# Kernel optimization log

Measured on AMD Instinct MI355X. Metric: run time of the kernel, lower is better.

Reference implementation:

```python
import jax, jax.numpy as jnp
import numpy as np
from functools import partial

DIM = 256
HEADS = 8
HEAD_DIM = DIM // HEADS
SCALES = (1, 2, 4)
B, H, W = 1, 64, 64


def _dwconv3x3(x, w, b):
    # x: (B,C,H,W), w: (C,1,3,3) depthwise, b: (C,)
    y = jax.lax.conv_general_dilated(
        x, w, window_strides=(1, 1), padding='SAME',
        feature_group_count=x.shape[1],
        dimension_numbers=('NCHW', 'OIHW', 'NCHW'))
    return y + b[None, :, None, None]


def _pwconv(x, w, b):
    # 1x1 conv: x (B,C,H,W), w (O,C), b (O,)
    return jnp.einsum('bchw,oc->bohw', x, w) + b[None, :, None, None]


def _avg_pool(x, s):
    Bb, C, Hh, Ww = x.shape
    return x.reshape(Bb, C, Hh // s, s, Ww // s, s).mean(axis=(3, 5))


def setup_inputs() -> dict:
    key = jax.random.key(0)
    ks = jax.random.split(key, 9)
    sc = 0.05
    return {
        'x': jax.random.normal(ks[0], (B, DIM, H, W), dtype=jnp.float32),
        'dw_w': jax.random.normal(ks[1], (3, DIM, 1, 3, 3), dtype=jnp.float32) * sc,
        'dw_b': jax.random.normal(ks[2], (3, DIM), dtype=jnp.float32) * sc,
        'pw_w': jax.random.normal(ks[3], (3, 3 * DIM, DIM), dtype=jnp.float32) * sc,
        'pw_b': jax.random.normal(ks[4], (3, 3 * DIM), dtype=jnp.float32) * sc,
        'pos_w': jax.random.normal(ks[5], (3, DIM, 1, 3, 3), dtype=jnp.float32) * sc,
        'pos_b': jax.random.normal(ks[6], (3, DIM), dtype=jnp.float32) * sc,
        'fusion_w': jax.random.normal(ks[7], (DIM, 3 * DIM), dtype=jnp.float32) * sc,
        'fusion_b': jax.random.normal(ks[8], (DIM,), dtype=jnp.float32) * sc,
    }


def reference(x, dw_w, dw_b, pw_w, pw_b, pos_w, pos_b, fusion_w, fusion_b):
    Bb, C, Hh, Ww = x.shape
    outputs = []
    for i, scale in enumerate(SCALES):
        xs = _avg_pool(x, scale) if scale > 1 else x
        # ConvQKV
        x_dw = _dwconv3x3(xs, dw_w[i], dw_b[i])
        qkv = _pwconv(x_dw, pw_w[i], pw_b[i])
        q, k, v = jnp.split(qkv, 3, axis=1)
        pos = _dwconv3x3(xs, pos_w[i], pos_b[i])
        q = q + pos
        k = k + pos
        Hs, Ws = xs.shape[2], xs.shape[3]
        Ns = Hs * Ws
        # (B, heads, head_dim, N)
        q = q.reshape(Bb, HEADS, HEAD_DIM, Ns)
        k = k.reshape(Bb, HEADS, HEAD_DIM, Ns)
        v = v.reshape(Bb, HEADS, HEAD_DIM, Ns)
        attn = jnp.einsum('bhdn,bhdm->bhnm', q, k) / (HEAD_DIM ** 0.5)
        attn = jax.nn.softmax(attn, axis=-1)
        out = jnp.einsum('bhnm,bhdm->bhdn', attn, v)  # (B,h,hd,N)
        out = out.reshape(Bb, C, Hs, Ws)
        if scale > 1:
            out = jax.image.resize(out, (Bb, C, Hh, Ww), method='bilinear')
        outputs.append(out)
    cat = jnp.concatenate(outputs, axis=1)  # (B, 3C, H, W)
    return jnp.einsum('bchw,oc->bohw', cat, fusion_w) + fusion_b[None, :, None, None]
```

## Files before the change

kernel.cpp:

```cpp
#include <hip/hip_runtime.h>
#include <math.h>

#define DIM 256
#define HEADS 8
#define HD 32
#define QSCALE 0.25504526770295183f

typedef __attribute__((ext_vector_type(8))) short bf16x8;
typedef __attribute__((ext_vector_type(4))) float f32x4;

#if __has_builtin(__builtin_amdgcn_exp2f)
#define EXP2(x) __builtin_amdgcn_exp2f(x)
#else
#define EXP2(x) __expf((x) * 0.6931471805599453f)
#endif

__device__ __forceinline__ unsigned short f2bf(float f) {
  unsigned int u = __float_as_uint(f);
  unsigned int r = u + 0x7fff + ((u >> 16) & 1);
  return (unsigned short)(r >> 16);
}
__device__ __forceinline__ float bf2f(unsigned short u) {
  return __uint_as_float(((unsigned int)u) << 16);
}


__global__ __launch_bounds__(256) void prep_kernel(const float* __restrict__ x,
    const float* __restrict__ pw_w, const float* __restrict__ fus_w,
    float* __restrict__ xs2, float* __restrict__ xs4,
    unsigned short* __restrict__ Wb, unsigned short* __restrict__ Wf) {
  const int gx = blockIdx.x, t = threadIdx.x;
  if (gx < 1024) {
    int id = gx * 256 + t;
    int c = id >> 10, n = id & 1023;
    int y = (n >> 5) << 1, x0 = (n & 31) << 1;
    const float* b = x + c * 4096 + y * 64 + x0;
    xs2[id] = (b[0] + b[1] + b[64] + b[65]) * 0.25f;
  } else if (gx < 1280) {
    int id = (gx - 1024) * 256 + t;
    int c = id >> 8, n = id & 255;
    int y = (n >> 4) << 2, x0 = (n & 15) << 2;
    const float* b = x + c * 4096 + y * 64 + x0;
    float s = 0.f;
    #pragma unroll
    for (int dy = 0; dy < 4; ++dy)
      #pragma unroll
      for (int dx = 0; dx < 4; ++dx) s += b[dy * 64 + dx];
    xs4[id] = s * 0.0625f;
  } else if (gx < 1424) {
    int lid = (gx - 1280) * 256 + t;
    int fb = lid >> 5, l = lid & 31;
    int scale = fb / 384, bs = fb - scale * 384;
    int rtile = bs >> 3, kchunk = bs & 7;
    int r = scale * 768 + rtile * 16 + (l & 7) * 2;
    int k = kchunk * 32 + (l >> 3) * 8;
    const float* s0 = pw_w + (size_t)r * 256 + k;
    float4 u0 = *(const float4*)(s0);
    float4 u1 = *(const float4*)(s0 + 4);
    float4 u2 = *(const float4*)(s0 + 256);
    float4 u3 = *(const float4*)(s0 + 260);
    unsigned short* d = Wb + (size_t)fb * 512 + l * 16;
    ushort4 a0 = {f2bf(u0.x), f2bf(u0.y), f2bf(u0.z), f2bf(u0.w)};
    ushort4 a1 = {f2bf(u1.x), f2bf(u1.y), f2bf(u1.z), f2bf(u1.w)};
    ushort4 a2 = {f2bf(u2.x), f2bf(u2.y), f2bf(u2.z), f2bf(u2.w)};
    ushort4 a3 = {f2bf(u3.x), f2bf(u3.y), f2bf(u3.z), f2bf(u3.w)};
    *(ushort4*)(d)      = a0;
    *(ushort4*)(d + 4)  = a1;
    *(ushort4*)(d + 8)  = a2;
    *(ushort4*)(d + 12) = a3;
  } else {
    int lid = (gx - 1424) * 256 + t;
    int fb = lid >> 5, l = lid & 31;
    int rtile = fb / 24, kchunk = fb - rtile * 24;
    int r = rtile * 16 + (l & 7) * 2;
    int k = kchunk * 32 + (l >> 3) * 8;
    const float* s0 = fus_w + (size_t)r * 768 + k;
    float4 u0 = *(const float4*)(s0);
    float4 u1 = *(const float4*)(s0 + 4);
    float4 u2 = *(const float4*)(s0 + 768);
    float4 u3 = *(const float4*)(s0 + 772);
    unsigned short* d = Wf + (size_t)fb * 512 + l * 16;
    ushort4 a0 = {f2bf(u0.x), f2bf(u0.y), f2bf(u0.z), f2bf(u0.w)};
    ushort4 a1 = {f2bf(u1.x), f2bf(u1.y), f2bf(u1.z), f2bf(u1.w)};
    ushort4 a2 = {f2bf(u2.x), f2bf(u2.y), f2bf(u2.z), f2bf(u2.w)};
    ushort4 a3 = {f2bf(u3.x), f2bf(u3.y), f2bf(u3.z), f2bf(u3.w)};
    *(ushort4*)(d)      = a0;
    *(ushort4*)(d + 4)  = a1;
    *(ushort4*)(d + 8)  = a2;
    *(ushort4*)(d + 12) = a3;
  }
}

__global__ __launch_bounds__(256) void dwt_kernel(const float* __restrict__ x,
    const float* __restrict__ xs2, const float* __restrict__ xs4,
    const float* __restrict__ dw_w, const float* __restrict__ dw_b,
    const float* __restrict__ pos_w, const float* __restrict__ pos_b,
    unsigned short* __restrict__ xdwT, unsigned short* __restrict__ posTc) {
  __shared__ __align__(16) unsigned short lds1[32][40];
  int b = blockIdx.x;
  const float* src;
  int lgHs, wo, soff;
  if (b < 1024)      { src = x;   lgHs = 6; wo = 0; soff = 0; }
  else if (b < 1280) { b -= 1024; src = xs2; lgHs = 5; wo = 1; soff = 1048576; }
  else               { b -= 1280; src = xs4; lgHs = 4; wo = 2; soff = 1310720; }
  const int c0 = (b & 7) * 32;
  const int n0 = (b >> 3) * 32;
  const int Hs = 1 << lgHs;
  const int Ns = Hs * Hs;
  const int t = threadIdx.x;
  const int cl = t >> 3;
  const int c = c0 + cl;
  const int nb = (t & 7) * 4;
  const float* w1 = dw_w + wo * 2304 + c * 9;
  const float* w2 = pos_w + wo * 2304 + c * 9;
  const float b1 = dw_b[wo * 256 + c], b2 = pos_b[wo * 256 + c];
  const int gn = n0 + nb;
  const int y = gn >> lgHs, xg = gn & (Hs - 1);
  const float* sc = src + c * Ns;
  float r[3][6];
  #pragma unroll
  for (int ky = 0; ky < 3; ++ky) {
    int yy = y + ky - 1;
    bool rok = (yy >= 0) && (yy < Hs);
    #pragma unroll
    for (int j = 0; j < 6; ++j) {
      int xx = xg - 1 + j;
      r[ky][j] = (rok && xx >= 0 && xx < Hs) ? sc[yy * Hs + xx] : 0.f;
    }
  }
  ushort4 pst;
  unsigned short* ps = (unsigned short*)&pst;
  #pragma unroll
  for (int i = 0; i < 4; ++i) {
    float s1 = b1, s2 = b2;
    #pragma unroll
    for (int ky = 0; ky < 3; ++ky)
      #pragma unroll
      for (int kx = 0; kx < 3; ++kx) {
        float v = r[ky][i + kx];
        s1 += v * w1[ky * 3 + kx];
        s2 += v * w2[ky * 3 + kx];
      }
    lds1[nb + i][cl] = f2bf(s1);
    ps[i] = f2bf(s2);
  }
  *(ushort4*)(posTc + soff + (size_t)c * Ns + gn) = pst;
  __syncthreads();
  if (t < 128) {
    int blk = t >> 6, l = t & 63;
    size_t bid = (size_t)((n0 >> 4) + blk) * 8 + (c0 >> 5);
    *(bf16x8*)(xdwT + soff + bid * 512 + (size_t)l * 8) =
        *(const bf16x8*)&lds1[blk * 16 + (l & 15)][(l >> 4) * 8];
  }
}

__global__ __launch_bounds__(256) void gemm_qkv_all(const unsigned short* __restrict__ WbA,
    const unsigned short* __restrict__ xdwTA, const float* __restrict__ biasA,
    const unsigned short* __restrict__ posTA, unsigned short* __restrict__ Qf,
    unsigned short* __restrict__ Kf, unsigned short* __restrict__ Vf) {
  int by = blockIdx.y;
  int Ns, off;
  const unsigned short *Wb, *xdwT, *posT;
  const float* bias;
  if (by < 64) {
    Ns = 4096; off = 0;
    Wb = WbA; bias = biasA;
  } else if (by < 80) {
    Ns = 1024; off = 1048576; by -= 64;
    Wb = WbA + 196608; bias = biasA + 768;
  } else {
    Ns = 256; off = 1310720; by -= 80;
    Wb = WbA + 393216; bias = biasA + 1536;
  }
  xdwT = xdwTA + off; posT = posTA + off;
  const int t = threadIdx.x;
  const int wave = t >> 6, lane = t & 63;
  const int ln = lane & 15, quad = lane >> 4;
  const int o0 = blockIdx.x * 64 + (wave & 1) * 32;
  const int n0 = by * 64 + (wave >> 1) * 32;
  const int at0 = (o0 >> 4) * 8, at1 = at0 + 8;
  const int bt0 = (n0 >> 4) * 8, bt1 = bt0 + 8;
  const bool vblk = blockIdx.x >= 8;
  f32x4 acc[2][2] = {};
  if (!vblk) {
    #pragma unroll
    for (int ks = 0; ks < 8; ++ks) {
      bf16x8 af0 = *(const bf16x8*)(Wb + (size_t)(at0 + ks) * 512 + lane * 8);
      bf16x8 af1 = *(const bf16x8*)(Wb + (size_t)(at1 + ks) * 512 + lane * 8);
      bf16x8 bv0 = *(const bf16x8*)(xdwT + (size_t)(bt0 + ks) * 512 + lane * 8);
      bf16x8 bv1 = *(const bf16x8*)(xdwT + (size_t)(bt1 + ks) * 512 + lane * 8);
      acc[0][0] = __builtin_amdgcn_mfma_f32_16x16x32_bf16(af0, bv0, acc[0][0], 0, 0, 0);
      acc[0][1] = __builtin_amdgcn_mfma_f32_16x16x32_bf16(af0, bv1, acc[0][1], 0, 0, 0);
      acc[1][0] = __builtin_amdgcn_mfma_f32_16x16x32_bf16(af1, bv0, acc[1][0], 0, 0, 0);
      acc[1][1] = __builtin_amdgcn_mfma_f32_16x16x32_bf16(af1, bv1, acc[1][1], 0, 0, 0);
    }
  } else {
    #pragma unroll
    for (int ks = 0; ks < 8; ++ks) {
      bf16x8 af0 = *(const bf16x8*)(Wb + (size_t)(at0 + ks) * 512 + lane * 8);
      bf16x8 af1 = *(const bf16x8*)(Wb + (size_t)(at1 + ks) * 512 + lane * 8);
      bf16x8 bv0 = *(const bf16x8*)(xdwT + (size_t)(bt0 + ks) * 512 + lane * 8);
      bf16x8 bv1 = *(const bf16x8*)(xdwT + (size_t)(bt1 + ks) * 512 + lane * 8);
      acc[0][0] = __builtin_amdgcn_mfma_f32_16x16x32_bf16(bv0, af0, acc[0][0], 0, 0, 0);
      acc[0][1] = __builtin_amdgcn_mfma_f32_16x16x32_bf16(bv0, af1, acc[0][1], 0, 0, 0);
      acc[1][0] = __builtin_amdgcn_mfma_f32_16x16x32_bf16(bv1, af0, acc[1][0], 0, 0, 0);
      acc[1][1] = __builtin_amdgcn_mfma_f32_16x16x32_bf16(bv1, af1, acc[1][1], 0, 0, 0);
    }
  }
  if (!vblk) {
    const int cat = blockIdx.x >> 2;
    #pragma unroll
    for (int mt = 0; mt < 2; ++mt) {
      int ot = o0 + mt * 16 + quad * 4;
      float bs0 = bias[ot], bs1 = bias[ot + 1], bs2 = bias[ot + 2], bs3 = bias[ot + 3];
      int cb = ot & 255;
      #pragma unroll
      for (int nt = 0; nt < 2; ++nt) {
        int nn = n0 + nt * 16 + ln;
        f32x4 v = acc[mt][nt];
        const unsigned short* pp = posT + (size_t)cb * Ns + nn;
        v.x += bs0 + bf2f(pp[0]);
        v.y += bs1 + bf2f(pp[Ns]);
        v.z += bs2 + bf2f(pp[2 * Ns]);
        v.w += bs3 + bf2f(pp[3 * Ns]);
        if (cat == 0) { v.x *= QSCALE; v.y *= QSCALE; v.z *= QSCALE; v.w *= QSCALE; }
        ushort4 st;
        st.x = f2bf(v.x); st.y = f2bf(v.y); st.z = f2bf(v.z); st.w = f2bf(v.w);
        int hh = cb >> 5, d = cb & 31;
        unsigned short* dst = (cat == 0 ? Qf : Kf) + off;
        size_t a = ((size_t)(hh * (Ns >> 4) + (nn >> 4)) * 64 + (d >> 3) * 16 + (nn & 15)) * 8
                   + (d & 7);
        *(ushort4*)(dst + a) = st;
      }
    }
  } else {
    #pragma unroll
    for (int a = 0; a < 2; ++a) {
      int nbase = n0 + a * 16 + quad * 4;
      #pragma unroll
      for (int bb = 0; bb < 2; ++bb) {
        int o = o0 + bb * 16 + ln;
        int c = o - 512;
        int hh = c >> 5, d = c & 31;
        int dt = d >> 4, dl = d & 15;
        float bs = bias[o];
        f32x4 v = acc[a][bb];
        ushort4 st;
        st.x = f2bf(v.x + bs); st.y = f2bf(v.y + bs);
        st.z = f2bf(v.z + bs); st.w = f2bf(v.w + bs);
        size_t adr = ((((size_t)hh * (Ns >> 5) + (nbase >> 5)) * 2 + dt) * 64
                      + ((nbase & 31) >> 3) * 16 + dl) * 8 + (nbase & 7);
        *(ushort4*)(Vf + off + adr) = st;
      }
    }
  }
}

__global__ __launch_bounds__(256) void attn_all_kernel(
    const unsigned short* __restrict__ Qf, const unsigned short* __restrict__ Kf,
    const unsigned short* __restrict__ Vf,
    unsigned short* __restrict__ accp1, unsigned short* __restrict__ p2,
    unsigned short* __restrict__ p4, float* __restrict__ ls1,
    float* __restrict__ ls2, float* __restrict__ ls4) {
  __shared__ unsigned short pt_lds[4 * 32 * 72];
  const int z = blockIdx.z;
  unsigned short* accp;
  float* lsump;
  int Ns, lgMs, sp, off;
  if (z < 8) {
    accp = accp1; lsump = ls1; Ns = 4096; lgMs = 9; sp = z; off = 0;
  } else if (z < 16) {
    if (blockIdx.x >= 8) return;
    accp = p2; lsump = ls2; Ns = 1024; lgMs = 7; sp = z - 8; off = 1048576;
  } else {
    if (blockIdx.x >= 2) return;
    accp = p4; lsump = ls4; Ns = 256; lgMs = 6; sp = z - 16; off = 1310720;
  }
  const int t = threadIdx.x;
  const int wave = t >> 6, lane = t & 63;
  const int ln = lane & 15, quad = lane >> 4;
  const int h = blockIdx.y;
  const int n0 = blockIdx.x * 128 + wave * 32;
  const unsigned short* qp = Qf + off
      + ((size_t)(h * (Ns >> 4) + (n0 >> 4)) * 64 + lane) * 8;
  bf16x8 qf0 = *(const bf16x8*)(qp);
  bf16x8 qf1 = *(const bf16x8*)(qp + 512);
  unsigned short* ptw = pt_lds + wave * (32 * 72);
  f32x4 acc[2][2] = {};
  f32x4 acc_l0 = {0.f, 0.f, 0.f, 0.f}, acc_l1 = {0.f, 0.f, 0.f, 0.f};
  const f32x4 zero = {0.f, 0.f, 0.f, 0.f};
  const short kOne = (short)0x3F80;
  const bf16x8 onesf = {kOne, kOne, kOne, kOne, kOne, kOne, kOne, kOne};
  const int m0s = sp << lgMs;
  const int nch = 1 << (lgMs - 6);
  const unsigned short* kp = Kf + off
      + ((size_t)(h * (Ns >> 4) + (m0s >> 4)) * 64 + lane) * 8;
  const unsigned short* vp = Vf + off
      + (((size_t)h * (Ns >> 5) + (m0s >> 5)) * 128 + lane) * 8;
  for (int ch = 0; ch < nch; ++ch) {
    const unsigned short* kc = kp + ch * 2048;
    const unsigned short* vc = vp + ch * 2048;
    bf16x8 kf0 = *(const bf16x8*)(kc);
    bf16x8 kf1 = *(const bf16x8*)(kc + 512);
    bf16x8 kf2 = *(const bf16x8*)(kc + 1024);
    bf16x8 kf3 = *(const bf16x8*)(kc + 1536);
    bf16x8 vf00 = *(const bf16x8*)(vc);
    bf16x8 vf10 = *(const bf16x8*)(vc + 512);
    bf16x8 vf01 = *(const bf16x8*)(vc + 1024);
    bf16x8 vf11 = *(const bf16x8*)(vc + 1536);
    f32x4 s[4][2];
    s[0][0] = __builtin_amdgcn_mfma_f32_16x16x32_bf16(kf0, qf0, zero, 0, 0, 0);
    s[0][1] = __builtin_amdgcn_mfma_f32_16x16x32_bf16(kf0, qf1, zero, 0, 0, 0);
    s[1][0] = __builtin_amdgcn_mfma_f32_16x16x32_bf16(kf1, qf0, zero, 0, 0, 0);
    s[1][1] = __builtin_amdgcn_mfma_f32_16x16x32_bf16(kf1, qf1, zero, 0, 0, 0);
    s[2][0] = __builtin_amdgcn_mfma_f32_16x16x32_bf16(kf2, qf0, zero, 0, 0, 0);
    s[2][1] = __builtin_amdgcn_mfma_f32_16x16x32_bf16(kf2, qf1, zero, 0, 0, 0);
    s[3][0] = __builtin_amdgcn_mfma_f32_16x16x32_bf16(kf3, qf0, zero, 0, 0, 0);
    s[3][1] = __builtin_amdgcn_mfma_f32_16x16x32_bf16(kf3, qf1, zero, 0, 0, 0);
    #pragma unroll
    for (int mt = 0; mt < 4; ++mt) {
      #pragma unroll
      for (int nt = 0; nt < 2; ++nt) {
        float e0 = EXP2(s[mt][nt].x);
        float e1 = EXP2(s[mt][nt].y);
        float e2 = EXP2(s[mt][nt].z);
        float e3 = EXP2(s[mt][nt].w);
        uint2 pk;
        pk.x = __builtin_amdgcn_perm(__float_as_uint(e1), __float_as_uint(e0), 0x07060302);
        pk.y = __builtin_amdgcn_perm(__float_as_uint(e3), __float_as_uint(e2), 0x07060302);
        *(uint2*)&ptw[(nt * 16 + ln) * 72 + mt * 16 + quad * 4] = pk;
      }
    }
    #pragma unroll
    for (int ks = 0; ks < 2; ++ks) {
      bf16x8 pf0 = *(const bf16x8*)&ptw[ln * 72 + ks * 32 + quad * 8];
      bf16x8 pf1 = *(const bf16x8*)&ptw[(16 + ln) * 72 + ks * 32 + quad * 8];
      bf16x8 va = ks ? vf01 : vf00;
      bf16x8 vbf = ks ? vf11 : vf10;
      acc[0][0] = __builtin_amdgcn_mfma_f32_16x16x32_bf16(va, pf0, acc[0][0], 0, 0, 0);
      acc[0][1] = __builtin_amdgcn_mfma_f32_16x16x32_bf16(va, pf1, acc[0][1], 0, 0, 0);
      acc[1][0] = __builtin_amdgcn_mfma_f32_16x16x32_bf16(vbf, pf0, acc[1][0], 0, 0, 0);
      acc[1][1] = __builtin_amdgcn_mfma_f32_16x16x32_bf16(vbf, pf1, acc[1][1], 0, 0, 0);
      acc_l0 = __builtin_amdgcn_mfma_f32_16x16x32_bf16(onesf, pf0, acc_l0, 0, 0, 0);
      acc_l1 = __builtin_amdgcn_mfma_f32_16x16x32_bf16(onesf, pf1, acc_l1, 0, 0, 0);
    }
  }
  unsigned short* ap = accp + ((size_t)sp * 256 + h * 32) * Ns;
  #pragma unroll
  for (int dt = 0; dt < 2; ++dt) {
    #pragma unroll
    for (int r = 0; r < 4; ++r) {
      int cl = dt * 16 + quad * 4 + r;
      ap[(size_t)cl * Ns + n0 + ln]      = f2bf(((const float*)&acc[dt][0])[r]);
      ap[(size_t)cl * Ns + n0 + 16 + ln] = f2bf(((const float*)&acc[dt][1])[r]);
    }
  }
  if (lane < 16) {
    float* lp = lsump + ((size_t)sp * 8 + h) * Ns + n0;
    lp[lane]      = acc_l0.x;
    lp[16 + lane] = acc_l1.x;
  }
}

__global__ __launch_bounds__(256) void combine24_kernel(const unsigned short* __restrict__ p2,
    const float* __restrict__ ls2, const unsigned short* __restrict__ p4,
    const float* __restrict__ ls4, float* __restrict__ out2, float* __restrict__ out4) {
  int id = blockIdx.x * 256 + threadIdx.x;
  if (id < 262144) {
    int n = id & 1023, h = id >> 15;
    float v = 0.f, d = 0.f;
    #pragma unroll
    for (int sp = 0; sp < 8; ++sp) {
      v += bf2f(p2[sp * 262144 + id]);
      d += ls2[sp * 8192 + h * 1024 + n];
    }
    out2[id] = v / d;
  } else {
    int idl = id - 262144;
    int n = idl & 255, h = idl >> 13;
    float v = 0.f, d = 0.f;
    #pragma unroll
    for (int sp = 0; sp < 4; ++sp) {
      v += bf2f(p4[sp * 65536 + idl]);
      d += ls4[sp * 2048 + h * 256 + n];
    }
    out4[idl] = v / d;
  }
}

__global__ __launch_bounds__(256) void build_catT_kernel(const unsigned short* __restrict__ accp,
    const float* __restrict__ lsum1, const float* __restrict__ out2,
    const float* __restrict__ out4, unsigned short* __restrict__ catT) {
  __shared__ unsigned short lds[64][72];
  const int t = threadIdx.x;
  const int n0 = blockIdx.x * 64;
  const int by = blockIdx.y;
  const int c0 = by * 64;
  if (by < 4) {
    #pragma unroll
    for (int p = 0; p < 4; ++p) {
      int ct = p * 16 + (t >> 4);
      int c = c0 + ct;
      int h = c >> 5;
      int nn = (t & 15) * 4;
      float vs[4] = {0.f, 0.f, 0.f, 0.f};
      float ds[4] = {0.f, 0.f, 0.f, 0.f};
      #pragma unroll
      for (int sp = 0; sp < 8; ++sp) {
        ushort4 a = *(const ushort4*)(accp + (size_t)sp * 1048576 + (size_t)c * 4096 + n0 + nn);
        vs[0] += bf2f(a.x); vs[1] += bf2f(a.y); vs[2] += bf2f(a.z); vs[3] += bf2f(a.w);
        float4 dd = *(const float4*)(lsum1 + (size_t)sp * 32768 + (size_t)h * 4096 + n0 + nn);
        ds[0] += dd.x; ds[1] += dd.y; ds[2] += dd.z; ds[3] += dd.w;
      }
      lds[nn + 0][ct] = f2bf(vs[0] / ds[0]);
      lds[nn + 1][ct] = f2bf(vs[1] / ds[1]);
      lds[nn + 2][ct] = f2bf(vs[2] / ds[2]);
      lds[nn + 3][ct] = f2bf(vs[3] / ds[3]);
    }
  } else {
    const bool s2 = by < 8;
    const float* src = s2 ? out2 : out4;
    const int Hs = s2 ? 32 : 16;
    const int coff = s2 ? 256 : 512;
    const float sc = (float)Hs / 64.0f;
    #pragma unroll
    for (int p = 0; p < 4; ++p) {
      int ct = p * 16 + (t >> 4);
      const float* s = src + (size_t)(c0 - coff + ct) * Hs * Hs;
      int nn = (t & 15) * 4;
      #pragma unroll
      for (int i = 0; i < 4; ++i) {
        int n = n0 + nn + i;
        int y = n >> 6, x = n & 63;
        float fy = ((float)y + 0.5f) * sc - 0.5f;
        float fx = ((float)x + 0.5f) * sc - 0.5f;
        float fy0 = floorf(fy), fx0 = floorf(fx);
        int y0 = (int)fy0, x0 = (int)fx0;
        float ty = fy - fy0, tx = fx - fx0;
        int y0c = min(max(y0, 0), Hs - 1), y1c = min(max(y0 + 1, 0), Hs - 1);
        int x0c = min(max(x0, 0), Hs - 1), x1c = min(max(x0 + 1, 0), Hs - 1);
        float v00 = s[y0c * Hs + x0c], v01 = s[y0c * Hs + x1c];
        float v10 = s[y1c * Hs + x0c], v11 = s[y1c * Hs + x1c];
        float v0 = v00 + (v01 - v00) * tx;
        float v1 = v10 + (v11 - v10) * tx;
        lds[nn + i][ct] = f2bf(v0 + (v1 - v0) * ty);
      }
    }
  }
  __syncthreads();
  int blk = t >> 5, l = t & 31;
  int ntile = blk >> 1, cchunk = blk & 1;
  int koct = l >> 3, r1 = (l & 7) * 2;
  size_t bid = (size_t)((n0 >> 4) + ntile) * 24 + (c0 >> 5) + cchunk;
  unsigned short* dst = catT + bid * 512 + (size_t)l * 16;
  *(bf16x8*)(dst)     = *(const bf16x8*)&lds[ntile * 16 + r1][cchunk * 32 + koct * 8];
  *(bf16x8*)(dst + 8) = *(const bf16x8*)&lds[ntile * 16 + r1 + 1][cchunk * 32 + koct * 8];
}

__global__ __launch_bounds__(256) void gemm_fus_mfma(const unsigned short* __restrict__ Wf,
    const unsigned short* __restrict__ catT, float* __restrict__ part) {
  const int t = threadIdx.x;
  const int wave = t >> 6, lane = t & 63;
  const int ln = lane & 15, quad = lane >> 4;
  const int o0 = blockIdx.x * 64 + (wave & 1) * 32;
  const int n0 = blockIdx.y * 64 + (wave >> 1) * 32;
  const int sp = blockIdx.z;
  const int at0 = (o0 >> 4) * 24 + sp * 8, at1 = at0 + 24;
  const int bt0 = (n0 >> 4) * 24 + sp * 8, bt1 = bt0 + 24;
  f32x4 acc[2][2] = {};
  #pragma unroll
  for (int ks = 0; ks < 8; ++ks) {
    bf16x8 af0 = *(const bf16x8*)(Wf + (size_t)(at0 + ks) * 512 + lane * 8);
    bf16x8 af1 = *(const bf16x8*)(Wf + (size_t)(at1 + ks) * 512 + lane * 8);
    bf16x8 bv0 = *(const bf16x8*)(catT + (size_t)(bt0 + ks) * 512 + lane * 8);
    bf16x8 bv1 = *(const bf16x8*)(catT + (size_t)(bt1 + ks) * 512 + lane * 8);
    acc[0][0] = __builtin_amdgcn_mfma_f32_16x16x32_bf16(bv0, af0, acc[0][0], 0, 0, 0);
    acc[0][1] = __builtin_amdgcn_mfma_f32_16x16x32_bf16(bv0, af1, acc[0][1], 0, 0, 0);
    acc[1][0] = __builtin_amdgcn_mfma_f32_16x16x32_bf16(bv1, af0, acc[1][0], 0, 0, 0);
    acc[1][1] = __builtin_amdgcn_mfma_f32_16x16x32_bf16(bv1, af1, acc[1][1], 0, 0, 0);
  }
  float* pp = part + (size_t)sp * 1048576;
  #pragma unroll
  for (int a = 0; a < 2; ++a) {
    int nbase = n0 + a * 16 + quad * 4;
    #pragma unroll
    for (int bb = 0; bb < 2; ++bb) {
      int o = o0 + bb * 16 + ln;
      float4 st;
      st.x = acc[a][bb].x; st.y = acc[a][bb].y; st.z = acc[a][bb].z; st.w = acc[a][bb].w;
      *(float4*)(pp + (size_t)o * 4096 + nbase) = st;
    }
  }
}

__global__ __launch_bounds__(256) void fus_combine_kernel(const float* __restrict__ part,
    const float* __restrict__ bias, float* __restrict__ out) {
  int id = blockIdx.x * 256 + threadIdx.x;
  int o = id >> 10;
  float4 v0 = *(const float4*)(part + id * 4);
  float4 v1 = *(const float4*)(part + 1048576 + id * 4);
  float4 v2 = *(const float4*)(part + 2097152 + id * 4);
  float bs = bias[o];
  float4 r;
  r.x = v0.x + v1.x + v2.x + bs;
  r.y = v0.y + v1.y + v2.y + bs;
  r.z = v0.z + v1.z + v2.z + bs;
  r.w = v0.w + v1.w + v2.w + bs;
  *(float4*)(out + id * 4) = r;
}

extern "C" void kernel_launch(void* const* d_in, const int* in_sizes, int n_in,
                              void* d_out, int out_size, void* d_ws, size_t ws_size,
                              hipStream_t stream) {
  const float* x     = (const float*)d_in[0];
  const float* dw_w  = (const float*)d_in[1];
  const float* dw_b  = (const float*)d_in[2];
  const float* pw_w  = (const float*)d_in[3];
  const float* pw_b  = (const float*)d_in[4];
  const float* pos_w = (const float*)d_in[5];
  const float* pos_b = (const float*)d_in[6];
  const float* fus_w = (const float*)d_in[7];
  const float* fus_b = (const float*)d_in[8];
  float* out = (float*)d_out;
  float* ws = (float*)d_ws;

  float* scratch = ws;
  float* posF   = ws + 1376256;
  float* accpF  = ws + 2752512;
  unsigned short* xdwT = (unsigned short*)(ws + 6946816);
  unsigned short* posTc = (unsigned short*)(ws + 7634944);
  unsigned short* Qf   = (unsigned short*)(ws + 8323072);
  unsigned short* Kf   = Qf + 1376256;
  unsigned short* Vf   = (unsigned short*)(ws + 9699328);
  unsigned short* catT = (unsigned short*)(ws + 10387456);
  unsigned short* Wf   = (unsigned short*)(ws + 11960320);

  float* xs2 = accpF;
  float* xs4 = accpF + 262144;
  unsigned short* Wb = catT;
  unsigned short* accp = (unsigned short*)accpF;
  float* lsump1 = posF;
  float* lsump2 = posF + 262144;
  float* lsump4 = posF + 327680;
  float* out2   = posF + 335872;
  float* out4   = posF + 598016;
  unsigned short* p2 = (unsigned short*)scratch;
  unsigned short* p4 = (unsigned short*)scratch + 2097152;
  float* part = accpF;

  prep_kernel<<<1472, 256, 0, stream>>>(x, pw_w, fus_w, xs2, xs4, Wb, Wf);
  dwt_kernel<<<1344, 256, 0, stream>>>(x, xs2, xs4, dw_w, dw_b, pos_w, pos_b, xdwT, posTc);
  gemm_qkv_all<<<dim3(12, 84), 256, 0, stream>>>(Wb, xdwT, pw_b, posTc, Qf, Kf, Vf);

  attn_all_kernel<<<dim3(32, 8, 20), 256, 0, stream>>>(Qf, Kf, Vf, accp, p2, p4,
                                                       lsump1, lsump2, lsump4);
  combine24_kernel<<<1280, 256, 0, stream>>>(p2, lsump2, p4, lsump4, out2, out4);

  build_catT_kernel<<<dim3(64, 12), 256, 0, stream>>>(accp, lsump1, out2, out4, catT);
  gemm_fus_mfma<<<dim3(4, 64, 3), 256, 0, stream>>>(Wf, catT, part);
  fus_combine_kernel<<<1024, 256, 0, stream>>>(part, fus_b, out);
}
```

Baseline: 148.2 us.

## Halve attention key splits and interleave exp with PV MFMAs per half-chunk

Cuts the number of key-dimension splits for scales 1 and 2 from 8 to 4, so each block covers twice as many keys. This halves the partial-result writes and the reduction reads in the combine and catT kernels, at the cost of fewer blocks (grid z drops from 20 to 12) and longer serial loops per block. It also splits the softmax-exp/LDS-store stage into two halves, issuing the PV MFMAs for the first half before computing exps for the second half, so exp and matrix work can overlap.

Result: no change. 146.8 us (-0.9%).

```diff
diff --git a/kernel.cpp b/kernel.cpp
--- a/kernel.cpp
+++ b/kernel.cpp
@@ -267,14 +267,14 @@
   unsigned short* accp;
   float* lsump;
   int Ns, lgMs, sp, off;
-  if (z < 8) {
-    accp = accp1; lsump = ls1; Ns = 4096; lgMs = 9; sp = z; off = 0;
-  } else if (z < 16) {
+  if (z < 4) {
+    accp = accp1; lsump = ls1; Ns = 4096; lgMs = 10; sp = z; off = 0;
+  } else if (z < 8) {
     if (blockIdx.x >= 8) return;
-    accp = p2; lsump = ls2; Ns = 1024; lgMs = 7; sp = z - 8; off = 1048576;
+    accp = p2; lsump = ls2; Ns = 1024; lgMs = 8; sp = z - 4; off = 1048576;
   } else {
     if (blockIdx.x >= 2) return;
-    accp = p4; lsump = ls4; Ns = 256; lgMs = 6; sp = z - 16; off = 1310720;
+    accp = p4; lsump = ls4; Ns = 256; lgMs = 6; sp = z - 8; off = 1310720;
   }
   const int t = threadIdx.x;
   const int wave = t >> 6, lane = t & 63;
@@ -318,7 +318,7 @@
     s[3][0] = __builtin_amdgcn_mfma_f32_16x16x32_bf16(kf3, qf0, zero, 0, 0, 0);
     s[3][1] = __builtin_amdgcn_mfma_f32_16x16x32_bf16(kf3, qf1, zero, 0, 0, 0);
     #pragma unroll
-    for (int mt = 0; mt < 4; ++mt) {
+    for (int mt = 0; mt < 2; ++mt) {
       #pragma unroll
       for (int nt = 0; nt < 2; ++nt) {
         float e0 = EXP2(s[mt][nt].x);
@@ -331,16 +331,37 @@
         *(uint2*)&ptw[(nt * 16 + ln) * 72 + mt * 16 + quad * 4] = pk;
       }
     }
-    #pragma unroll
-    for (int ks = 0; ks < 2; ++ks) {
-      bf16x8 pf0 = *(const bf16x8*)&ptw[ln * 72 + ks * 32 + quad * 8];
-      bf16x8 pf1 = *(const bf16x8*)&ptw[(16 + ln) * 72 + ks * 32 + quad * 8];
-      bf16x8 va = ks ? vf01 : vf00;
-      bf16x8 vbf = ks ? vf11 : vf10;
-      acc[0][0] = __builtin_amdgcn_mfma_f32_16x16x32_bf16(va, pf0, acc[0][0], 0, 0, 0);
-      acc[0][1] = __builtin_amdgcn_mfma_f32_16x16x32_bf16(va, pf1, acc[0][1], 0, 0, 0);
-      acc[1][0] = __builtin_amdgcn_mfma_f32_16x16x32_bf16(vbf, pf0, acc[1][0], 0, 0, 0);
-      acc[1][1] = __builtin_amdgcn_mfma_f32_16x16x32_bf16(vbf, pf1, acc[1][1], 0, 0, 0);
+    {
+      bf16x8 pf0 = *(const bf16x8*)&ptw[ln * 72 + quad * 8];
+      bf16x8 pf1 = *(const bf16x8*)&ptw[(16 + ln) * 72 + quad * 8];
+      acc[0][0] = __builtin_amdgcn_mfma_f32_16x16x32_bf16(vf00, pf0, acc[0][0], 0, 0, 0);
+      acc[0][1] = __builtin_amdgcn_mfma_f32_16x16x32_bf16(vf00, pf1, acc[0][1], 0, 0, 0);
+      acc[1][0] = __builtin_amdgcn_mfma_f32_16x16x32_bf16(vf10, pf0, acc[1][0], 0, 0, 0);
+      acc[1][1] = __builtin_amdgcn_mfma_f32_16x16x32_bf16(vf10, pf1, acc[1][1], 0, 0, 0);
+      acc_l0 = __builtin_amdgcn_mfma_f32_16x16x32_bf16(onesf, pf0, acc_l0, 0, 0, 0);
+      acc_l1 = __builtin_amdgcn_mfma_f32_16x16x32_bf16(onesf, pf1, acc_l1, 0, 0, 0);
+    }
+    #pragma unroll
+    for (int mt = 2; mt < 4; ++mt) {
+      #pragma unroll
+      for (int nt = 0; nt < 2; ++nt) {
+        float e0 = EXP2(s[mt][nt].x);
+        float e1 = EXP2(s[mt][nt].y);
+        float e2 = EXP2(s[mt][nt].z);
+        float e3 = EXP2(s[mt][nt].w);
+        uint2 pk;
+        pk.x = __builtin_amdgcn_perm(__float_as_uint(e1), __float_as_uint(e0), 0x07060302);
+        pk.y = __builtin_amdgcn_perm(__float_as_uint(e3), __float_as_uint(e2), 0x07060302);
+        *(uint2*)&ptw[(nt * 16 + ln) * 72 + mt * 16 + quad * 4] = pk;
+      }
+    }
+    {
+      bf16x8 pf0 = *(const bf16x8*)&ptw[ln * 72 + 32 + quad * 8];
+      bf16x8 pf1 = *(const bf16x8*)&ptw[(16 + ln) * 72 + 32 + quad * 8];
+      acc[0][0] = __builtin_amdgcn_mfma_f32_16x16x32_bf16(vf01, pf0, acc[0][0], 0, 0, 0);
+      acc[0][1] = __builtin_amdgcn_mfma_f32_16x16x32_bf16(vf01, pf1, acc[0][1], 0, 0, 0);
+      acc[1][0] = __builtin_amdgcn_mfma_f32_16x16x32_bf16(vf11, pf0, acc[1][0], 0, 0, 0);
+      acc[1][1] = __builtin_amdgcn_mfma_f32_16x16x32_bf16(vf11, pf1, acc[1][1], 0, 0, 0);
       acc_l0 = __builtin_amdgcn_mfma_f32_16x16x32_bf16(onesf, pf0, acc_l0, 0, 0, 0);
       acc_l1 = __builtin_amdgcn_mfma_f32_16x16x32_bf16(onesf, pf1, acc_l1, 0, 0, 0);
     }
@@ -370,7 +391,7 @@
     int n = id & 1023, h = id >> 15;
     float v = 0.f, d = 0.f;
     #pragma unroll
-    for (int sp = 0; sp < 8; ++sp) {
+    for (int sp = 0; sp < 4; ++sp) {
       v += bf2f(p2[sp * 262144 + id]);
       d += ls2[sp * 8192 + h * 1024 + n];
     }
@@ -406,7 +427,7 @@
       float vs[4] = {0.f, 0.f, 0.f, 0.f};
       float ds[4] = {0.f, 0.f, 0.f, 0.f};
       #pragma unroll
-      for (int sp = 0; sp < 8; ++sp) {
+      for (int sp = 0; sp < 4; ++sp) {
         ushort4 a = *(const ushort4*)(accp + (size_t)sp * 1048576 + (size_t)c * 4096 + n0 + nn);
         vs[0] += bf2f(a.x); vs[1] += bf2f(a.y); vs[2] += bf2f(a.z); vs[3] += bf2f(a.w);
         float4 dd = *(const float4*)(lsum1 + (size_t)sp * 32768 + (size_t)h * 4096 + n0 + nn);
@@ -552,7 +573,7 @@
   dwt_kernel<<<1344, 256, 0, stream>>>(x, xs2, xs4, dw_w, dw_b, pos_w, pos_b, xdwT, posTc);
   gemm_qkv_all<<<dim3(12, 84), 256, 0, stream>>>(Wb, xdwT, pw_b, posTc, Qf, Kf, Vf);
 
-  attn_all_kernel<<<dim3(32, 8, 20), 256, 0, stream>>>(Qf, Kf, Vf, accp, p2, p4,
+  attn_all_kernel<<<dim3(32, 8, 12), 256, 0, stream>>>(Qf, Kf, Vf, accp, p2, p4,
                                                        lsump1, lsump2, lsump4);
   combine24_kernel<<<1280, 256, 0, stream>>>(p2, lsump2, p4, lsump4, out2, out4);
 
```
